# Performance work log

Measured on AMD Instinct MI355X. Metric: run time of the kernel, lower is better.

## Reference

```python
import jax, jax.numpy as jnp
import numpy as np

B, C, H, W = 2048, 4, 84, 84
FEAT = 7 * 7 * 64  # 3136, from 84->20->9->7 conv arithmetic
D = 512
E = 6            # num_experts
K = 2            # top_k
A = 12           # output_dim (actions)


def _conv(x, w, b, stride):
    y = jax.lax.conv_general_dilated(
        x, w, window_strides=(stride, stride), padding='VALID',
        dimension_numbers=('NCHW', 'OIHW', 'NCHW'))
    return y + b[None, :, None, None]


def setup_inputs() -> dict:
    key = jax.random.key(0)
    ks = jax.random.split(key, 16)
    s = lambda k, shape, fan: jax.random.normal(k, shape, jnp.float32) * (1.0 / np.sqrt(fan))
    return {
        'x': jax.random.normal(ks[0], (B, C, H, W), jnp.float32),
        'c1_w': s(ks[1], (32, C, 8, 8), C * 64), 'c1_b': jnp.zeros((32,), jnp.float32),
        'c2_w': s(ks[2], (64, 32, 4, 4), 32 * 16), 'c2_b': jnp.zeros((64,), jnp.float32),
        'c3_w': s(ks[3], (64, 64, 3, 3), 64 * 9), 'c3_b': jnp.zeros((64,), jnp.float32),
        'fc_w': s(ks[4], (FEAT, D), FEAT), 'fc_b': jnp.zeros((D,), jnp.float32),
        'gate_w': s(ks[5], (D, E), D), 'gate_b': jnp.zeros((E,), jnp.float32),
        'e_w1': s(ks[6], (E, D, D), D), 'e_b1': jnp.zeros((E, D), jnp.float32),
        'e_w2': s(ks[7], (E, D, D), D), 'e_b2': jnp.zeros((E, D), jnp.float32),
        'e_w3': s(ks[8], (E, D, A), D), 'e_b3': jnp.zeros((E, A), jnp.float32),
    }


def reference(x, c1_w, c1_b, c2_w, c2_b, c3_w, c3_b, fc_w, fc_b,
              gate_w, gate_b, e_w1, e_b1, e_w2, e_b2, e_w3, e_b3):
    # CNN feature extractor (dropout omitted: eval semantics)
    h = jax.nn.relu(_conv(x, c1_w, c1_b, 4))
    h = jax.nn.relu(_conv(h, c2_w, c2_b, 2))
    h = jax.nn.relu(_conv(h, c3_w, c3_b, 1))
    h = h.reshape(h.shape[0], -1)                     # [B, 3136] (C,H,W flatten order)
    f = jax.nn.relu(h @ fc_w + fc_b)                  # [B, 512]

    # Gating: softmax -> top-2 -> renormalize
    gate_probs = jax.nn.softmax(f @ gate_w + gate_b, axis=-1)    # [B, E]
    top_p, top_i = jax.lax.top_k(gate_probs, K)                   # [B, K]
    top_p = top_p / jnp.sum(top_p, axis=-1, keepdims=True)

    # Experts: compute all (tiny MLPs), then gather top-k outputs
    h1 = jax.nn.relu(jnp.einsum('bd,edh->beh', f, e_w1) + e_b1)   # [B, E, D]
    h2 = jax.nn.relu(jnp.einsum('beh,ehg->beg', h1, e_w2) + e_b2) # [B, E, D]
    eo = jnp.einsum('beg,ego->beo', h2, e_w3) + e_b3              # [B, E, A]
    sel = jnp.take_along_axis(eo, top_i[:, :, None], axis=1)      # [B, K, A]
    out = jnp.sum(sel * top_p[:, :, None], axis=1)                # [B, A]
    return out
```

## Files before the change

kernel.cpp:

```cpp
#include <hip/hip_runtime.h>
#include <hip/hip_bf16.h>
#include <math.h>

typedef __attribute__((ext_vector_type(8))) short bf16x8;
typedef __attribute__((ext_vector_type(4))) float f32x4;

__device__ __forceinline__ float b2f(unsigned short u) {
    unsigned int v = ((unsigned int)u) << 16;
    return __uint_as_float(v);
}
__device__ __forceinline__ unsigned short f2b(float f) {
    __hip_bfloat16 h = __float2bfloat16(f);
    return *reinterpret_cast<unsigned short*>(&h);
}

__global__ __launch_bounds__(256) void prep_w(
    const float* __restrict__ w1, const float* __restrict__ w2, const float* __restrict__ w3,
    float* __restrict__ w1r, unsigned short* __restrict__ w2h, unsigned short* __restrict__ w2l,
    unsigned short* __restrict__ w3h, unsigned short* __restrict__ w3l) {
    int tid = blockIdx.x * 256 + threadIdx.x;
    if (tid < 8192) {
        int k = tid >> 8, r = tid & 255;
        int c = r >> 6, ky = (r >> 3) & 7, kx = r & 7;
        w1r[((ky * 4 + c) * 8 + kx) * 32 + k] = w1[tid];
    } else if (tid < 8192 + 32768) {
        int i = tid - 8192;
        int n = i >> 9, r = i & 511;
        int c = r >> 4, ky = (r >> 2) & 3, kx = r & 3;
        float v = w2[i];
        unsigned short h = f2b(v);
        int d = ((ky * 4 + kx) * 64 + n) * 32 + c;
        w2h[d] = h;
        w2l[d] = f2b(v - b2f(h));
    } else if (tid < 8192 + 32768 + 36864) {
        int i = tid - 40960;
        int n = i / 576, r = i - n * 576;
        int c = r / 9, s = r - c * 9;
        int ky = s / 3, kx = s - ky * 3;
        float v = w3[i];
        unsigned short h = f2b(v);
        int d = (((ky * 3 + kx) * 2 + (c >> 5)) * 64 + n) * 32 + (c & 31);
        w3h[d] = h;
        w3l[d] = f2b(v - b2f(h));
    }
}

__global__ __launch_bounds__(256) void prep_fcw(
    const float* __restrict__ fw, unsigned short* __restrict__ h, unsigned short* __restrict__ l) {
    __shared__ float tile[64][65];
    int k0 = blockIdx.x * 64;
    int n0 = blockIdx.y * 64;
    int tx = threadIdx.x & 63, ty = threadIdx.x >> 6;
#pragma unroll
    for (int j = 0; j < 16; j++) {
        int kk = ty + j * 4;
        int kp = k0 + kk;
        int p = kp >> 6, c = kp & 63;
        tile[kk][tx] = fw[(c * 49 + p) * 512 + n0 + tx];
    }
    __syncthreads();
#pragma unroll
    for (int j = 0; j < 16; j++) {
        int r = ty + j * 4;
        float v = tile[tx][r];
        unsigned short hh = f2b(v);
        long d = (long)(n0 + r) * 3136 + k0 + tx;
        h[d] = hh;
        l[d] = f2b(v - b2f(hh));
    }
}

__global__ __launch_bounds__(256) void prep_ewT(
    const float* __restrict__ ew1, const float* __restrict__ ew2,
    unsigned short* __restrict__ t1, unsigned short* __restrict__ t2) {
    __shared__ float tile[32][33];
    int z = blockIdx.z;
    int e = z % 6;
    const float* src = (z < 6) ? (ew1 + e * 262144) : (ew2 + e * 262144);
    unsigned short* dst = (z < 6) ? (t1 + e * 262144) : (t2 + e * 262144);
    int d0 = blockIdx.y * 32;
    int h0 = blockIdx.x * 32;
    int tx = threadIdx.x, ty = threadIdx.y;
#pragma unroll
    for (int j = 0; j < 4; j++)
        tile[ty + j * 8][tx] = src[(d0 + ty + j * 8) * 512 + h0 + tx];
    __syncthreads();
#pragma unroll
    for (int j = 0; j < 4; j++)
        dst[(h0 + ty + j * 8) * 512 + (d0 + tx)] = f2b(tile[tx][ty + j * 8]);
}

__global__ __launch_bounds__(256) void conv1_k(
    const float* __restrict__ x, const float* __restrict__ w1r,
    const float* __restrict__ b1, unsigned short* __restrict__ yhi,
    unsigned short* __restrict__ ylo) {
    int px = blockIdx.x * 256 + threadIdx.x;
    int n = px / 400;
    int rem = px - n * 400;
    int oy = rem / 20;
    int ox = rem - oy * 20;
    const float* xb = x + (long)n * 28224 + oy * 4 * 84 + ox * 4;
    float acc[32];
#pragma unroll
    for (int k = 0; k < 32; k++) acc[k] = b1[k];
    for (int ky = 0; ky < 8; ky++) {
        const float* xr = xb + ky * 84;
        float4 xv[8];
#pragma unroll
        for (int c = 0; c < 4; c++) {
            xv[c * 2]     = *(const float4*)(xr + c * 7056);
            xv[c * 2 + 1] = *(const float4*)(xr + c * 7056 + 4);
        }
        const float* wk = w1r + ky * 1024;
#pragma unroll
        for (int c = 0; c < 4; c++) {
            float xs[8] = {xv[c * 2].x,     xv[c * 2].y,     xv[c * 2].z,     xv[c * 2].w,
                           xv[c * 2 + 1].x, xv[c * 2 + 1].y, xv[c * 2 + 1].z, xv[c * 2 + 1].w};
#pragma unroll
            for (int kx = 0; kx < 8; kx++) {
                float xsv = xs[kx];
                const float* w = wk + (c * 8 + kx) * 32;
#pragma unroll
                for (int k = 0; k < 32; k++) acc[k] = fmaf(xsv, w[k], acc[k]);
            }
        }
    }
    long o = (long)px * 32;
#pragma unroll
    for (int g = 0; g < 4; g++) {
        bf16x8 hv, lv;
#pragma unroll
        for (int j = 0; j < 8; j++) {
            float v = fmaxf(acc[g * 8 + j], 0.f);
            unsigned short h = f2b(v);
            hv[j] = (short)h;
            lv[j] = (short)f2b(v - b2f(h));
        }
        *(bf16x8*)(yhi + o + g * 8) = hv;
        *(bf16x8*)(ylo + o + g * 8) = lv;
    }
}

template <int C, int IH, int IW, int OH, int OW, int S, int KH, int KW>
__global__ __launch_bounds__(256) void convm_k(
    const unsigned short* __restrict__ xhi, const unsigned short* __restrict__ xlo,
    const unsigned short* __restrict__ whi, const unsigned short* __restrict__ wlo,
    const float* __restrict__ bias,
    unsigned short* __restrict__ yhi, unsigned short* __restrict__ ylo) {
    constexpr int CH = C / 32;
    constexpr int NCHUNK = KH * KW * CH;
    __shared__ unsigned short Ah[256][40], Al[256][40], Bh[64][40], Bl[64][40];
    int t = threadIdx.x;
    int px = blockIdx.x * 256 + t;
    int n = px / (OH * OW);
    int rem = px - n * (OH * OW);
    int oy = rem / OW;
    int ox = rem - oy * OW;
    const long xoff = (((long)n * IH + oy * S) * IW + ox * S) * C;
    int wave = t >> 6, lane = t & 63, l16 = lane & 15, quad = lane >> 4;
    int br = t >> 2, bc = (t & 3) * 8;
    f32x4 acc[4][4];
#pragma unroll
    for (int i = 0; i < 4; i++)
#pragma unroll
        for (int j = 0; j < 4; j++)
#pragma unroll
            for (int r = 0; r < 4; r++) acc[i][j][r] = 0.f;
    for (int ck = 0; ck < NCHUNK; ck++) {
        int kyx = ck / CH;
        int ch = ck - kyx * CH;
        int ky = kyx / KW, kx = kyx - ky * KW;
        long a_src = xoff + ((ky * IW + kx) * C + ch * 32);
#pragma unroll
        for (int j = 0; j < 4; j++) {
            *(bf16x8*)&Ah[t][j * 8] = *(const bf16x8*)(xhi + a_src + j * 8);
            *(bf16x8*)&Al[t][j * 8] = *(const bf16x8*)(xlo + a_src + j * 8);
        }
        long b_src = (long)ck * 2048 + br * 32 + bc;
        *(bf16x8*)&Bh[br][bc] = *(const bf16x8*)(whi + b_src);
        *(bf16x8*)&Bl[br][bc] = *(const bf16x8*)(wlo + b_src);
        __syncthreads();
        bf16x8 ah[4], al[4], bh[4], bl[4];
#pragma unroll
        for (int i = 0; i < 4; i++) {
            ah[i] = *(const bf16x8*)&Ah[wave * 64 + i * 16 + l16][quad * 8];
            al[i] = *(const bf16x8*)&Al[wave * 64 + i * 16 + l16][quad * 8];
            bh[i] = *(const bf16x8*)&Bh[i * 16 + l16][quad * 8];
            bl[i] = *(const bf16x8*)&Bl[i * 16 + l16][quad * 8];
        }
#pragma unroll
        for (int i = 0; i < 4; i++)
#pragma unroll
            for (int j = 0; j < 4; j++) {
                acc[i][j] = __builtin_amdgcn_mfma_f32_16x16x32_bf16(ah[i], bh[j], acc[i][j], 0, 0, 0);
                acc[i][j] = __builtin_amdgcn_mfma_f32_16x16x32_bf16(ah[i], bl[j], acc[i][j], 0, 0, 0);
                acc[i][j] = __builtin_amdgcn_mfma_f32_16x16x32_bf16(al[i], bh[j], acc[i][j], 0, 0, 0);
            }
        __syncthreads();
    }
    int pxbase = blockIdx.x * 256 + wave * 64;
#pragma unroll
    for (int i = 0; i < 4; i++)
#pragma unroll
        for (int j = 0; j < 4; j++) {
            int col = j * 16 + l16;
            float bv = bias[col];
#pragma unroll
            for (int r = 0; r < 4; r++) {
                int prow = pxbase + i * 16 + quad * 4 + r;
                float v = fmaxf(acc[i][j][r] + bv, 0.f);
                unsigned short h = f2b(v);
                yhi[(long)prow * 64 + col] = h;
                ylo[(long)prow * 64 + col] = f2b(v - b2f(h));
            }
        }
}

__global__ __launch_bounds__(256) void fc_k(
    const unsigned short* __restrict__ Ahi, const unsigned short* __restrict__ Alo,
    const unsigned short* __restrict__ Bhi, const unsigned short* __restrict__ Blo,
    const float* __restrict__ bias, float* __restrict__ Cf, unsigned short* __restrict__ Cb) {
    __shared__ unsigned short Ash[64][40], Asl[64][40], Bsh[64][40], Bsl[64][40];
    int t = threadIdx.x;
    int m0 = blockIdx.x * 64, n0 = blockIdx.y * 64;
    int wave = t >> 6, lane = t & 63, l16 = lane & 15, quad = lane >> 4;
    int wm = (wave & 1) * 32, wn = (wave >> 1) * 32;
    int sr = t >> 2, sk = (t & 3) * 8;
    f32x4 acc[2][2];
#pragma unroll
    for (int i = 0; i < 2; i++)
#pragma unroll
        for (int j = 0; j < 2; j++)
#pragma unroll
            for (int r = 0; r < 4; r++) acc[i][j][r] = 0.f;
    for (int k0 = 0; k0 < 3136; k0 += 32) {
        *(bf16x8*)&Ash[sr][sk] = *(const bf16x8*)(Ahi + (long)(m0 + sr) * 3136 + k0 + sk);
        *(bf16x8*)&Asl[sr][sk] = *(const bf16x8*)(Alo + (long)(m0 + sr) * 3136 + k0 + sk);
        *(bf16x8*)&Bsh[sr][sk] = *(const bf16x8*)(Bhi + (long)(n0 + sr) * 3136 + k0 + sk);
        *(bf16x8*)&Bsl[sr][sk] = *(const bf16x8*)(Blo + (long)(n0 + sr) * 3136 + k0 + sk);
        __syncthreads();
        bf16x8 ah[2], al[2], bh[2], bl[2];
#pragma unroll
        for (int i = 0; i < 2; i++) {
            ah[i] = *(const bf16x8*)&Ash[wm + i * 16 + l16][quad * 8];
            al[i] = *(const bf16x8*)&Asl[wm + i * 16 + l16][quad * 8];
            bh[i] = *(const bf16x8*)&Bsh[wn + i * 16 + l16][quad * 8];
            bl[i] = *(const bf16x8*)&Bsl[wn + i * 16 + l16][quad * 8];
        }
#pragma unroll
        for (int i = 0; i < 2; i++)
#pragma unroll
            for (int j = 0; j < 2; j++) {
                acc[i][j] = __builtin_amdgcn_mfma_f32_16x16x32_bf16(ah[i], bh[j], acc[i][j], 0, 0, 0);
                acc[i][j] = __builtin_amdgcn_mfma_f32_16x16x32_bf16(ah[i], bl[j], acc[i][j], 0, 0, 0);
                acc[i][j] = __builtin_amdgcn_mfma_f32_16x16x32_bf16(al[i], bh[j], acc[i][j], 0, 0, 0);
            }
        __syncthreads();
    }
#pragma unroll
    for (int mt = 0; mt < 2; mt++)
#pragma unroll
        for (int nt = 0; nt < 2; nt++) {
            int col = n0 + wn + nt * 16 + l16;
            float bcol = bias[col];
#pragma unroll
            for (int r = 0; r < 4; r++) {
                int row = m0 + wm + mt * 16 + quad * 4 + r;
                float v = fmaxf(acc[mt][nt][r] + bcol, 0.f);
                Cf[row * 512 + col] = v;
                Cb[row * 512 + col] = f2b(v);
            }
        }
}

__global__ __launch_bounds__(256) void gate_k(
    const float* __restrict__ f, const float* __restrict__ gw, const float* __restrict__ gb,
    int* __restrict__ topi, float* __restrict__ topp) {
    int wave = threadIdx.x >> 6, lane = threadIdx.x & 63;
    int row = blockIdx.x * 4 + wave;
    float fv[8];
#pragma unroll
    for (int j = 0; j < 8; j++) fv[j] = f[row * 512 + lane + 64 * j];
    float lg[6];
#pragma unroll
    for (int e = 0; e < 6; e++) {
        float a = 0.f;
#pragma unroll
        for (int j = 0; j < 8; j++) a += fv[j] * gw[(lane + 64 * j) * 6 + e];
#pragma unroll
        for (int off = 32; off > 0; off >>= 1) a += __shfl_xor(a, off, 64);
        lg[e] = a + gb[e];
    }
    if (lane == 0) {
        int i1 = 0;
        float v1 = lg[0];
#pragma unroll
        for (int e = 1; e < 6; e++)
            if (lg[e] > v1) { v1 = lg[e]; i1 = e; }
        int i2 = (i1 == 0) ? 1 : 0;
        float v2 = lg[i2];
#pragma unroll
        for (int e = 0; e < 6; e++)
            if (e != i1 && lg[e] > v2) { v2 = lg[e]; i2 = e; }
        float pa = 1.f / (1.f + expf(v2 - v1));
        topi[row * 2] = i1;
        topi[row * 2 + 1] = i2;
        topp[row * 2] = pa;
        topp[row * 2 + 1] = 1.f - pa;
    }
}

__global__ __launch_bounds__(256) void moe_gemm(
    const unsigned short* __restrict__ A, long aStride,
    const unsigned short* __restrict__ Bt, const float* __restrict__ bias,
    unsigned short* __restrict__ C) {
    int e = blockIdx.z;
    const unsigned short* Ae = A + (long)e * aStride;
    const unsigned short* Be = Bt + (long)e * 262144;
    const float* be = bias + e * 512;
    unsigned short* Ce = C + (long)e * 2048 * 512;
    __shared__ unsigned short As[64 * 40];
    __shared__ unsigned short Bs[64 * 40];
    int t = threadIdx.x;
    int m0 = blockIdx.x * 64, n0 = blockIdx.y * 64;
    int wave = t >> 6, lane = t & 63;
    int l16 = lane & 15, quad = lane >> 4;
    int wm = (wave & 1) * 32, wn = (wave >> 1) * 32;
    int sm = t >> 2, sk = (t & 3) * 8;
    f32x4 acc[2][2];
#pragma unroll
    for (int i = 0; i < 2; i++)
#pragma unroll
        for (int j = 0; j < 2; j++)
#pragma unroll
            for (int r = 0; r < 4; r++) acc[i][j][r] = 0.f;
    for (int k0 = 0; k0 < 512; k0 += 32) {
        bf16x8 av = *(const bf16x8*)&Ae[(long)(m0 + sm) * 512 + k0 + sk];
        bf16x8 bv = *(const bf16x8*)&Be[(long)(n0 + sm) * 512 + k0 + sk];
        *(bf16x8*)&As[sm * 40 + sk] = av;
        *(bf16x8*)&Bs[sm * 40 + sk] = bv;
        __syncthreads();
        bf16x8 af0 = *(const bf16x8*)&As[(wm + l16) * 40 + quad * 8];
        bf16x8 af1 = *(const bf16x8*)&As[(wm + 16 + l16) * 40 + quad * 8];
        bf16x8 bf0 = *(const bf16x8*)&Bs[(wn + l16) * 40 + quad * 8];
        bf16x8 bf1 = *(const bf16x8*)&Bs[(wn + 16 + l16) * 40 + quad * 8];
        acc[0][0] = __builtin_amdgcn_mfma_f32_16x16x32_bf16(af0, bf0, acc[0][0], 0, 0, 0);
        acc[0][1] = __builtin_amdgcn_mfma_f32_16x16x32_bf16(af0, bf1, acc[0][1], 0, 0, 0);
        acc[1][0] = __builtin_amdgcn_mfma_f32_16x16x32_bf16(af1, bf0, acc[1][0], 0, 0, 0);
        acc[1][1] = __builtin_amdgcn_mfma_f32_16x16x32_bf16(af1, bf1, acc[1][1], 0, 0, 0);
        __syncthreads();
    }
#pragma unroll
    for (int mt = 0; mt < 2; mt++)
#pragma unroll
        for (int nt = 0; nt < 2; nt++) {
            int col = n0 + wn + nt * 16 + l16;
            float bcol = be[col];
#pragma unroll
            for (int r = 0; r < 4; r++) {
                int row = m0 + wm + mt * 16 + quad * 4 + r;
                float v = fmaxf(acc[mt][nt][r] + bcol, 0.f);
                Ce[(long)row * 512 + col] = f2b(v);
            }
        }
}

__global__ __launch_bounds__(256) void combine_k(
    const unsigned short* __restrict__ h2, const float* __restrict__ w3,
    const float* __restrict__ b3, const int* __restrict__ topi,
    const float* __restrict__ topp, float* __restrict__ out) {
    int tid = blockIdx.x * 256 + threadIdx.x;
    if (tid >= 2048 * 12) return;
    int b = tid / 12, a = tid % 12;
    float r = 0.f;
#pragma unroll
    for (int j = 0; j < 2; j++) {
        int e = topi[b * 2 + j];
        float p = topp[b * 2 + j];
        const unsigned short* h = h2 + ((long)e * 2048 + b) * 512;
        const float* w = w3 + e * 512 * 12 + a;
        float acc = b3[e * 12 + a];
#pragma unroll 4
        for (int k = 0; k < 512; k++) acc += b2f(h[k]) * w[k * 12];
        r += p * acc;
    }
    out[tid] = r;
}

extern "C" void kernel_launch(void* const* d_in, const int* in_sizes, int n_in,
                              void* d_out, int out_size, void* d_ws, size_t ws_size,
                              hipStream_t stream) {
    const float* x   = (const float*)d_in[0];
    const float* c1w = (const float*)d_in[1];
    const float* c1b = (const float*)d_in[2];
    const float* c2w = (const float*)d_in[3];
    const float* c2b = (const float*)d_in[4];
    const float* c3w = (const float*)d_in[5];
    const float* c3b = (const float*)d_in[6];
    const float* fcw = (const float*)d_in[7];
    const float* fcb = (const float*)d_in[8];
    const float* gw  = (const float*)d_in[9];
    const float* gb  = (const float*)d_in[10];
    const float* ew1 = (const float*)d_in[11];
    const float* eb1 = (const float*)d_in[12];
    const float* ew2 = (const float*)d_in[13];
    const float* eb2 = (const float*)d_in[14];
    const float* ew3 = (const float*)d_in[15];
    const float* eb3 = (const float*)d_in[16];

    char* ws = (char*)d_ws;
    unsigned short* y1hi = (unsigned short*)(ws + 0L);
    unsigned short* y1lo = (unsigned short*)(ws + 52428800L);
    unsigned short* f3hi = (unsigned short*)(ws + 0L);
    unsigned short* f3lo = (unsigned short*)(ws + 12845056L);
    unsigned short* y2hi = (unsigned short*)(ws + 104857600L);
    unsigned short* y2lo = (unsigned short*)(ws + 126091264L);
    unsigned short* h1   = (unsigned short*)(ws + 104857600L);
    unsigned short* h2   = (unsigned short*)(ws + 117440512L);
    float* f             = (float*)(ws + 147324928L);
    unsigned short* fb   = (unsigned short*)(ws + 151519232L);
    int*   topi          = (int*)(ws + 153616384L);
    float* topp          = (float*)(ws + 153632768L);
    float* w1r           = (float*)(ws + 153649152L);
    unsigned short* w2h  = (unsigned short*)(ws + 153681920L);
    unsigned short* w2l  = (unsigned short*)(ws + 153747456L);
    unsigned short* w3h  = (unsigned short*)(ws + 153812992L);
    unsigned short* w3l  = (unsigned short*)(ws + 153886720L);
    unsigned short* fcwh = (unsigned short*)(ws + 153960448L);
    unsigned short* fcwl = (unsigned short*)(ws + 157171712L);
    unsigned short* ew1t = (unsigned short*)(ws + 160382976L);
    unsigned short* ew2t = (unsigned short*)(ws + 163528704L);
    float* out = (float*)d_out;

    hipLaunchKernelGGL(prep_w, dim3(304), dim3(256), 0, stream, c1w, c2w, c3w, w1r, w2h, w2l, w3h, w3l);
    hipLaunchKernelGGL(prep_fcw, dim3(49, 8), dim3(256), 0, stream, fcw, fcwh, fcwl);
    hipLaunchKernelGGL(prep_ewT, dim3(16, 16, 12), dim3(32, 8), 0, stream, ew1, ew2, ew1t, ew2t);
    hipLaunchKernelGGL(conv1_k, dim3(3200), dim3(256), 0, stream, x, w1r, c1b, y1hi, y1lo);
    hipLaunchKernelGGL((convm_k<32, 20, 20, 9, 9, 2, 4, 4>), dim3(648), dim3(256), 0, stream,
                       y1hi, y1lo, w2h, w2l, c2b, y2hi, y2lo);
    hipLaunchKernelGGL((convm_k<64, 9, 9, 7, 7, 1, 3, 3>), dim3(392), dim3(256), 0, stream,
                       y2hi, y2lo, w3h, w3l, c3b, f3hi, f3lo);
    hipLaunchKernelGGL(fc_k, dim3(32, 8), dim3(256), 0, stream, f3hi, f3lo, fcwh, fcwl, fcb, f, fb);
    hipLaunchKernelGGL(gate_k, dim3(512), dim3(256), 0, stream, f, gw, gb, topi, topp);
    hipLaunchKernelGGL(moe_gemm, dim3(32, 8, 6), dim3(256), 0, stream, fb, 0L, ew1t, eb1, h1);
    hipLaunchKernelGGL(moe_gemm, dim3(32, 8, 6), dim3(256), 0, stream, h1, 1048576L, ew2t, eb2, h2);
    hipLaunchKernelGGL(combine_k, dim3(96), dim3(256), 0, stream, h2, ew3, eb3, topi, topp, out);
}
```

Baseline: 852.4 us.

## Move conv1 to split-bf16 MFMA, split-K the FC GEMM, vectorize expert combine

Conv1 moves from scalar FP32 FMAs to bf16 MFMA. Inputs are split into hi/lo bf16 by truncation, and three MFMAs per tile keep near-FP32 accuracy. The FC GEMM is split along K into two halves written to a partial buffer, followed by a new finish kernel that sums them and applies bias and ReLU, to raise occupancy on the 256-block grid. The combine kernel now uses one wave per batch row, a transposed expert-3 weight, vector loads and shuffle reductions instead of a scalar loop over 512 per output. This adds an extra kernel launch and partial-sum traffic.

```diff
diff --git a/kernel.cpp b/kernel.cpp
--- a/kernel.cpp
+++ b/kernel.cpp
@@ -13,16 +13,29 @@
     __hip_bfloat16 h = __float2bfloat16(f);
     return *reinterpret_cast<unsigned short*>(&h);
 }
+__device__ __forceinline__ void split_trunc(float v, short& h, short& l) {
+    unsigned int ui = __float_as_uint(v);
+    h = (short)(ui >> 16);
+    float hf = __uint_as_float(ui & 0xffff0000u);
+    l = (short)f2b(v - hf);
+}
 
 __global__ __launch_bounds__(256) void prep_w(
     const float* __restrict__ w1, const float* __restrict__ w2, const float* __restrict__ w3,
-    float* __restrict__ w1r, unsigned short* __restrict__ w2h, unsigned short* __restrict__ w2l,
-    unsigned short* __restrict__ w3h, unsigned short* __restrict__ w3l) {
+    const float* __restrict__ ew3,
+    unsigned short* __restrict__ wb1h, unsigned short* __restrict__ wb1l,
+    unsigned short* __restrict__ w2h, unsigned short* __restrict__ w2l,
+    unsigned short* __restrict__ w3h, unsigned short* __restrict__ w3l,
+    float* __restrict__ w3t) {
     int tid = blockIdx.x * 256 + threadIdx.x;
     if (tid < 8192) {
         int k = tid >> 8, r = tid & 255;
         int c = r >> 6, ky = (r >> 3) & 7, kx = r & 7;
-        w1r[((ky * 4 + c) * 8 + kx) * 32 + k] = w1[tid];
+        float v = w1[tid];
+        unsigned short h = f2b(v);
+        int d = ((ky * 2 + (k >> 4)) * 16 + (k & 15)) * 32 + c * 8 + kx;
+        wb1h[d] = h;
+        wb1l[d] = f2b(v - b2f(h));
     } else if (tid < 8192 + 32768) {
         int i = tid - 8192;
         int n = i >> 9, r = i & 511;
@@ -42,6 +55,11 @@
         int d = (((ky * 3 + kx) * 2 + (c >> 5)) * 64 + n) * 32 + (c & 31);
         w3h[d] = h;
         w3l[d] = f2b(v - b2f(h));
+    } else if (tid < 77824 + 36864) {
+        int i = tid - 77824;
+        int e = i / 6144, rem = i - e * 6144;
+        int a = rem >> 9, k = rem & 511;
+        w3t[i] = ew3[e * 6144 + k * 12 + a];
     }
 }
 
@@ -91,53 +109,78 @@
 }
 
 __global__ __launch_bounds__(256) void conv1_k(
-    const float* __restrict__ x, const float* __restrict__ w1r,
-    const float* __restrict__ b1, unsigned short* __restrict__ yhi,
-    unsigned short* __restrict__ ylo) {
-    int px = blockIdx.x * 256 + threadIdx.x;
-    int n = px / 400;
-    int rem = px - n * 400;
-    int oy = rem / 20;
-    int ox = rem - oy * 20;
-    const float* xb = x + (long)n * 28224 + oy * 4 * 84 + ox * 4;
-    float acc[32];
-#pragma unroll
-    for (int k = 0; k < 32; k++) acc[k] = b1[k];
+    const float* __restrict__ x, const unsigned short* __restrict__ wbh,
+    const unsigned short* __restrict__ wbl, const float* __restrict__ b1,
+    unsigned short* __restrict__ yhi, unsigned short* __restrict__ ylo) {
+    int t = threadIdx.x;
+    int wave = t >> 6, lane = t & 63, l16 = lane & 15, quad = lane >> 4;
+    int px0 = blockIdx.x * 256 + wave * 64;
+    const float* abase[4];
+#pragma unroll
+    for (int i = 0; i < 4; i++) {
+        int px = px0 + i * 16 + l16;
+        int n = px / 400;
+        int rem = px - n * 400;
+        int oy = rem / 20;
+        int ox = rem - oy * 20;
+        abase[i] = x + (long)n * 28224 + quad * 7056 + oy * 4 * 84 + ox * 4;
+    }
+    f32x4 acc[4][2];
+#pragma unroll
+    for (int i = 0; i < 4; i++)
+#pragma unroll
+        for (int j = 0; j < 2; j++)
+#pragma unroll
+            for (int r = 0; r < 4; r++) acc[i][j][r] = 0.f;
+#pragma unroll
     for (int ky = 0; ky < 8; ky++) {
-        const float* xr = xb + ky * 84;
-        float4 xv[8];
-#pragma unroll
-        for (int c = 0; c < 4; c++) {
-            xv[c * 2]     = *(const float4*)(xr + c * 7056);
-            xv[c * 2 + 1] = *(const float4*)(xr + c * 7056 + 4);
-        }
-        const float* wk = w1r + ky * 1024;
-#pragma unroll
-        for (int c = 0; c < 4; c++) {
-            float xs[8] = {xv[c * 2].x,     xv[c * 2].y,     xv[c * 2].z,     xv[c * 2].w,
-                           xv[c * 2 + 1].x, xv[c * 2 + 1].y, xv[c * 2 + 1].z, xv[c * 2 + 1].w};
-#pragma unroll
-            for (int kx = 0; kx < 8; kx++) {
-                float xsv = xs[kx];
-                const float* w = wk + (c * 8 + kx) * 32;
-#pragma unroll
-                for (int k = 0; k < 32; k++) acc[k] = fmaf(xsv, w[k], acc[k]);
+        bf16x8 ah[4], al[4];
+#pragma unroll
+        for (int i = 0; i < 4; i++) {
+            const float* p = abase[i] + ky * 84;
+            float4 v0 = *(const float4*)p;
+            float4 v1 = *(const float4*)(p + 4);
+            float v[8] = {v0.x, v0.y, v0.z, v0.w, v1.x, v1.y, v1.z, v1.w};
+#pragma unroll
+            for (int j = 0; j < 8; j++) {
+                short hh, ll;
+                split_trunc(v[j], hh, ll);
+                ah[i][j] = hh;
+                al[i][j] = ll;
             }
         }
-    }
-    long o = (long)px * 32;
-#pragma unroll
-    for (int g = 0; g < 4; g++) {
-        bf16x8 hv, lv;
-#pragma unroll
-        for (int j = 0; j < 8; j++) {
-            float v = fmaxf(acc[g * 8 + j], 0.f);
-            unsigned short h = f2b(v);
-            hv[j] = (short)h;
-            lv[j] = (short)f2b(v - b2f(h));
-        }
-        *(bf16x8*)(yhi + o + g * 8) = hv;
-        *(bf16x8*)(ylo + o + g * 8) = lv;
+        int wo = (ky * 2 * 16 + l16) * 32 + quad * 8;
+        bf16x8 bh0 = *(const bf16x8*)(wbh + wo);
+        bf16x8 bh1 = *(const bf16x8*)(wbh + wo + 512);
+        bf16x8 bl0 = *(const bf16x8*)(wbl + wo);
+        bf16x8 bl1 = *(const bf16x8*)(wbl + wo + 512);
+#pragma unroll
+        for (int i = 0; i < 4; i++) {
+            acc[i][0] = __builtin_amdgcn_mfma_f32_16x16x32_bf16(ah[i], bh0, acc[i][0], 0, 0, 0);
+            acc[i][0] = __builtin_amdgcn_mfma_f32_16x16x32_bf16(al[i], bh0, acc[i][0], 0, 0, 0);
+            acc[i][0] = __builtin_amdgcn_mfma_f32_16x16x32_bf16(ah[i], bl0, acc[i][0], 0, 0, 0);
+            acc[i][1] = __builtin_amdgcn_mfma_f32_16x16x32_bf16(ah[i], bh1, acc[i][1], 0, 0, 0);
+            acc[i][1] = __builtin_amdgcn_mfma_f32_16x16x32_bf16(al[i], bh1, acc[i][1], 0, 0, 0);
+            acc[i][1] = __builtin_amdgcn_mfma_f32_16x16x32_bf16(ah[i], bl1, acc[i][1], 0, 0, 0);
+        }
+    }
+    float bias0 = b1[l16], bias1 = b1[16 + l16];
+#pragma unroll
+    for (int i = 0; i < 4; i++) {
+#pragma unroll
+        for (int r = 0; r < 4; r++) {
+            long px = px0 + i * 16 + quad * 4 + r;
+            long o = px * 32;
+            float v0 = fmaxf(acc[i][0][r] + bias0, 0.f);
+            float v1 = fmaxf(acc[i][1][r] + bias1, 0.f);
+            short h0, l0, h1, l1;
+            split_trunc(v0, h0, l0);
+            split_trunc(v1, h1, l1);
+            yhi[o + l16] = (unsigned short)h0;
+            ylo[o + l16] = (unsigned short)l0;
+            yhi[o + 16 + l16] = (unsigned short)h1;
+            ylo[o + 16 + l16] = (unsigned short)l1;
+        }
     }
 }
 
@@ -219,10 +262,12 @@
 __global__ __launch_bounds__(256) void fc_k(
     const unsigned short* __restrict__ Ahi, const unsigned short* __restrict__ Alo,
     const unsigned short* __restrict__ Bhi, const unsigned short* __restrict__ Blo,
-    const float* __restrict__ bias, float* __restrict__ Cf, unsigned short* __restrict__ Cb) {
+    float* __restrict__ Cp) {
     __shared__ unsigned short Ash[64][40], Asl[64][40], Bsh[64][40], Bsl[64][40];
     int t = threadIdx.x;
     int m0 = blockIdx.x * 64, n0 = blockIdx.y * 64;
+    int z = blockIdx.z;
+    int kBase = z * 1568;
     int wave = t >> 6, lane = t & 63, l16 = lane & 15, quad = lane >> 4;
     int wm = (wave & 1) * 32, wn = (wave >> 1) * 32;
     int sr = t >> 2, sk = (t & 3) * 8;
@@ -233,7 +278,7 @@
         for (int j = 0; j < 2; j++)
 #pragma unroll
             for (int r = 0; r < 4; r++) acc[i][j][r] = 0.f;
-    for (int k0 = 0; k0 < 3136; k0 += 32) {
+    for (int k0 = kBase; k0 < kBase + 1568; k0 += 32) {
         *(bf16x8*)&Ash[sr][sk] = *(const bf16x8*)(Ahi + (long)(m0 + sr) * 3136 + k0 + sk);
         *(bf16x8*)&Asl[sr][sk] = *(const bf16x8*)(Alo + (long)(m0 + sr) * 3136 + k0 + sk);
         *(bf16x8*)&Bsh[sr][sk] = *(const bf16x8*)(Bhi + (long)(n0 + sr) * 3136 + k0 + sk);
@@ -257,20 +302,29 @@
             }
         __syncthreads();
     }
+    float* Cz = Cp + (long)z * 1048576;
 #pragma unroll
     for (int mt = 0; mt < 2; mt++)
 #pragma unroll
         for (int nt = 0; nt < 2; nt++) {
             int col = n0 + wn + nt * 16 + l16;
-            float bcol = bias[col];
 #pragma unroll
             for (int r = 0; r < 4; r++) {
                 int row = m0 + wm + mt * 16 + quad * 4 + r;
-                float v = fmaxf(acc[mt][nt][r] + bcol, 0.f);
-                Cf[row * 512 + col] = v;
-                Cb[row * 512 + col] = f2b(v);
+                Cz[row * 512 + col] = acc[mt][nt][r];
             }
         }
+}
+
+__global__ __launch_bounds__(256) void fc_fin(
+    const float* __restrict__ Cp, const float* __restrict__ bias,
+    float* __restrict__ f, unsigned short* __restrict__ fb) {
+    int tid = blockIdx.x * 256 + threadIdx.x;
+    int col = tid & 511;
+    float v = Cp[tid] + Cp[tid + 1048576] + bias[col];
+    v = fmaxf(v, 0.f);
+    f[tid] = v;
+    fb[tid] = f2b(v);
 }
 
 __global__ __launch_bounds__(256) void gate_k(
@@ -366,25 +420,45 @@
 }
 
 __global__ __launch_bounds__(256) void combine_k(
-    const unsigned short* __restrict__ h2, const float* __restrict__ w3,
+    const unsigned short* __restrict__ h2, const float* __restrict__ w3t,
     const float* __restrict__ b3, const int* __restrict__ topi,
     const float* __restrict__ topp, float* __restrict__ out) {
-    int tid = blockIdx.x * 256 + threadIdx.x;
-    if (tid >= 2048 * 12) return;
-    int b = tid / 12, a = tid % 12;
-    float r = 0.f;
+    int b = blockIdx.x * 4 + (threadIdx.x >> 6);
+    int lane = threadIdx.x & 63;
+    int e0 = topi[b * 2], e1 = topi[b * 2 + 1];
+    float p0 = topp[b * 2], p1 = topp[b * 2 + 1];
+    float r[12];
+#pragma unroll
+    for (int a = 0; a < 12; a++) r[a] = 0.f;
 #pragma unroll
     for (int j = 0; j < 2; j++) {
-        int e = topi[b * 2 + j];
-        float p = topp[b * 2 + j];
-        const unsigned short* h = h2 + ((long)e * 2048 + b) * 512;
-        const float* w = w3 + e * 512 * 12 + a;
-        float acc = b3[e * 12 + a];
-#pragma unroll 4
-        for (int k = 0; k < 512; k++) acc += b2f(h[k]) * w[k * 12];
-        r += p * acc;
-    }
-    out[tid] = r;
+        int e = j ? e1 : e0;
+        float p = j ? p1 : p0;
+        const unsigned short* hp = h2 + ((long)e * 2048 + b) * 512 + lane * 8;
+        bf16x8 hv = *(const bf16x8*)hp;
+        float hf[8];
+#pragma unroll
+        for (int q = 0; q < 8; q++) hf[q] = b2f((unsigned short)hv[q]);
+        const float* wb = w3t + e * 6144 + lane * 8;
+#pragma unroll
+        for (int a = 0; a < 12; a++) {
+            float4 w0 = *(const float4*)(wb + a * 512);
+            float4 w1 = *(const float4*)(wb + a * 512 + 4);
+            float acc = hf[0] * w0.x + hf[1] * w0.y + hf[2] * w0.z + hf[3] * w0.w +
+                        hf[4] * w1.x + hf[5] * w1.y + hf[6] * w1.z + hf[7] * w1.w;
+            r[a] += p * acc;
+        }
+    }
+#pragma unroll
+    for (int a = 0; a < 12; a++)
+#pragma unroll
+        for (int off = 32; off > 0; off >>= 1) r[a] += __shfl_xor(r[a], off, 64);
+    float v = 0.f;
+#pragma unroll
+    for (int a = 0; a < 12; a++)
+        if (lane == a) v = r[a];
+    if (lane < 12)
+        out[b * 12 + lane] = v + p0 * b3[e0 * 12 + lane] + p1 * b3[e1 * 12 + lane];
 }
 
 extern "C" void kernel_launch(void* const* d_in, const int* in_sizes, int n_in,
@@ -421,7 +495,6 @@
     unsigned short* fb   = (unsigned short*)(ws + 151519232L);
     int*   topi          = (int*)(ws + 153616384L);
     float* topp          = (float*)(ws + 153632768L);
-    float* w1r           = (float*)(ws + 153649152L);
     unsigned short* w2h  = (unsigned short*)(ws + 153681920L);
     unsigned short* w2l  = (unsigned short*)(ws + 153747456L);
     unsigned short* w3h  = (unsigned short*)(ws + 153812992L);
@@ -430,19 +503,25 @@
     unsigned short* fcwl = (unsigned short*)(ws + 157171712L);
     unsigned short* ew1t = (unsigned short*)(ws + 160382976L);
     unsigned short* ew2t = (unsigned short*)(ws + 163528704L);
+    float* w3t           = (float*)(ws + 166674432L);
+    float* Cp            = (float*)(ws + 166821888L);
+    unsigned short* wb1h = (unsigned short*)(ws + 175210496L);
+    unsigned short* wb1l = (unsigned short*)(ws + 175226880L);
     float* out = (float*)d_out;
 
-    hipLaunchKernelGGL(prep_w, dim3(304), dim3(256), 0, stream, c1w, c2w, c3w, w1r, w2h, w2l, w3h, w3l);
+    hipLaunchKernelGGL(prep_w, dim3(448), dim3(256), 0, stream, c1w, c2w, c3w, ew3,
+                       wb1h, wb1l, w2h, w2l, w3h, w3l, w3t);
     hipLaunchKernelGGL(prep_fcw, dim3(49, 8), dim3(256), 0, stream, fcw, fcwh, fcwl);
     hipLaunchKernelGGL(prep_ewT, dim3(16, 16, 12), dim3(32, 8), 0, stream, ew1, ew2, ew1t, ew2t);
-    hipLaunchKernelGGL(conv1_k, dim3(3200), dim3(256), 0, stream, x, w1r, c1b, y1hi, y1lo);
+    hipLaunchKernelGGL(conv1_k, dim3(3200), dim3(256), 0, stream, x, wb1h, wb1l, c1b, y1hi, y1lo);
     hipLaunchKernelGGL((convm_k<32, 20, 20, 9, 9, 2, 4, 4>), dim3(648), dim3(256), 0, stream,
                        y1hi, y1lo, w2h, w2l, c2b, y2hi, y2lo);
     hipLaunchKernelGGL((convm_k<64, 9, 9, 7, 7, 1, 3, 3>), dim3(392), dim3(256), 0, stream,
                        y2hi, y2lo, w3h, w3l, c3b, f3hi, f3lo);
-    hipLaunchKernelGGL(fc_k, dim3(32, 8), dim3(256), 0, stream, f3hi, f3lo, fcwh, fcwl, fcb, f, fb);
+    hipLaunchKernelGGL(fc_k, dim3(32, 8, 2), dim3(256), 0, stream, f3hi, f3lo, fcwh, fcwl, Cp);
+    hipLaunchKernelGGL(fc_fin, dim3(4096), dim3(256), 0, stream, Cp, fcb, f, fb);
     hipLaunchKernelGGL(gate_k, dim3(512), dim3(256), 0, stream, f, gw, gb, topi, topp);
     hipLaunchKernelGGL(moe_gemm, dim3(32, 8, 6), dim3(256), 0, stream, fb, 0L, ew1t, eb1, h1);
     hipLaunchKernelGGL(moe_gemm, dim3(32, 8, 6), dim3(256), 0, stream, h1, 1048576L, ew2t, eb2, h2);
-    hipLaunchKernelGGL(combine_k, dim3(96), dim3(256), 0, stream, h2, ew3, eb3, topi, topp, out);
-}
+    hipLaunchKernelGGL(combine_k, dim3(512), dim3(256), 0, stream, h2, w3t, eb3, topi, topp, out);
+}
```

After: 715.1 us. 1.19x faster.
